# Optimization experiments

Hardware: AMD Instinct MI355X
Metric: run time of the kernel (lower is better)

## Reference

```python
import jax, jax.numpy as jnp
import numpy as np

N = 50000          # nodes per type (assmpt=0, non_assmpt=1, rule=2)
E = 400000         # edges per relation
# (src_type, dst_type) for the 9 relations in the module's dict order
REL = [(0, 2), (1, 2), (1, 0), (0, 0), (2, 1), (2, 0), (0, 0), (2, 2), (1, 1)]


def setup_inputs() -> dict:
    key = jax.random.key(0)
    ks = jax.random.split(key, 8)
    inp = {
        "x_assmpt": jax.random.normal(ks[0], (N, 128), jnp.float32),
        "x_non_assmpt": jax.random.normal(ks[1], (N, 128), jnp.float32),
        "x_rule": jax.random.normal(ks[2], (N, 128), jnp.float32),
        "W1": jax.random.normal(ks[3], (9, 128, 128), jnp.float32) * 0.06,
        "b1": jnp.zeros((9, 128), jnp.float32),
        "W2": jax.random.normal(ks[4], (9, 128, 128), jnp.float32) * 0.06,
        "b2": jnp.zeros((9, 128), jnp.float32),
        "Wc": jax.random.normal(ks[5], (128, 16), jnp.float32) * 0.08,
        "bc": jnp.zeros((16,), jnp.float32),
        "edges": jax.random.randint(ks[6], (9, 2, E), 0, N, jnp.int32),
    }
    return inp


def _hetero_layer(xs, edges, W, b):
    """One HeteroGraphConv layer (DGL GraphConv, norm='both', aggregate='sum').
    xs: list of 3 [N, din]; W: [9, din, dout]; b: [9, dout]. Returns list of 3 [N, dout]."""
    dout = W.shape[2]
    outs = [jnp.zeros((N, dout), xs[0].dtype) for _ in range(3)]
    for r, (s, d) in enumerate(REL):
        src, dst = edges[r, 0], edges[r, 1]
        ones = jnp.ones((E,), xs[0].dtype)
        out_deg = jax.ops.segment_sum(ones, src, num_segments=N)   # src out-degree
        in_deg = jax.ops.segment_sum(ones, dst, num_segments=N)    # dst in-degree
        norm_s = jnp.where(out_deg > 0, out_deg, 1.0) ** -0.5
        norm_s = jnp.where(out_deg > 0, norm_s, 0.0)
        norm_d = jnp.where(in_deg > 0, in_deg, 1.0) ** -0.5
        norm_d = jnp.where(in_deg > 0, norm_d, 0.0)
        h = (xs[s] * norm_s[:, None]) @ W[r]                       # [N, dout] project first
        agg = jax.ops.segment_sum(h[src], dst, num_segments=N)     # SpMM gather/scatter
        outs[d] = outs[d] + agg * norm_d[:, None] + b[r]
    return outs


def reference(x_assmpt, x_non_assmpt, x_rule, W1, b1, W2, b2, Wc, bc, edges):
    xs = [x_assmpt, x_non_assmpt, x_rule]
    h = _hetero_layer(xs, edges, W1, b1)
    h = [jax.nn.relu(v) for v in h]
    h = _hetero_layer(h, edges, W2, b2)
    h = [jax.nn.relu(v) for v in h]
    h = [v @ Wc + bc for v in h]
    return jnp.stack(h, axis=0)  # [3, N, out] : (assmpt, non_assmpt, rule)
```

## Files before the change

kernel.cpp:

```cpp
#include <hip/hip_runtime.h>
#include <hip/hip_bf16.h>
#include <hip/hip_fp16.h>


#define NN 50000
#define EE 400000
#define NRG 4
#define RGN (NN / NRG)
#define HCH 16
#define HEG (EE / HCH)
#define NBK 98
#define BKW 512
#define CH1 8192
#define NCH ((EE + CH1 - 1) / CH1)
#define SCAP 6656

typedef __attribute__((ext_vector_type(8))) _Float16 f16x8;
typedef __attribute__((ext_vector_type(4))) float f32x4;
#define MFMAH(a, b, c) __builtin_amdgcn_mfma_f32_16x16x32_f16(a, b, c, 0, 0, 0)

__global__ __launch_bounds__(256) void k_hist(const int* __restrict__ edges,
                                              unsigned* __restrict__ hist) {
    __shared__ unsigned bins[RGN / 2];
    int bid = blockIdx.x;
    int r = bid >> 6;
    int rem = bid & 63;
    int rg = rem >> 4;
    int c = rem & 15;
    int tid = threadIdx.x;
    for (int i = tid; i < RGN / 2; i += 256) bins[i] = 0;
    __syncthreads();
    const int* ea = edges + (size_t)r * 2 * EE + (size_t)c * HEG;
    int base = rg * RGN;
    for (int e = tid; e < HEG; e += 256) {
        int idx = __builtin_nontemporal_load(&ea[e]) - base;
        if ((unsigned)idx < (unsigned)RGN)
            atomicAdd(&bins[idx >> 1], (idx & 1) ? 65536u : 1u);
    }
    __syncthreads();
    unsigned* ho = hist + ((size_t)(r * NRG + rg) * HCH + c) * (RGN / 2);
    for (int i = tid; i < RGN / 2; i += 256) ho[i] = bins[i];
}

__global__ void k_sums(const unsigned* __restrict__ hist, float* __restrict__ ns) {
    int i = blockIdx.x * blockDim.x + threadIdx.x;
    if (i >= 9 * (NN / 2)) return;
    int r = i / (NN / 2);
    int ps = i - r * (NN / 2);
    int rg = ps / (RGN / 2);
    int slot = ps - rg * (RGN / 2);
    const unsigned* hs = hist + ((size_t)(r * NRG + rg) * HCH) * (RGN / 2) + slot;
    unsigned slo = 0, shi = 0;
#pragma unroll
    for (int c = 0; c < HCH; ++c) {
        unsigned a = hs[(size_t)c * (RGN / 2)];
        slo += a & 0xffffu; shi += a >> 16;
    }
    int n0 = 2 * ps;
    ns[r * NN + n0]     = slo ? rsqrtf((float)slo) : 0.f;
    ns[r * NN + n0 + 1] = shi ? rsqrtf((float)shi) : 0.f;
}

__global__ __launch_bounds__(256) void k_bcount(const int* __restrict__ edges,
                                                int* __restrict__ bcount) {
    __shared__ int bins[NBK];
    int bid = blockIdx.x;
    int r = bid / NCH, c = bid - r * NCH;
    int tid = threadIdx.x;
    for (int i = tid; i < NBK; i += 256) bins[i] = 0;
    __syncthreads();
    int e0 = c * CH1, e1 = min(EE, e0 + CH1);
    const int* ed = edges + (size_t)r * 2 * EE + EE;
    for (int e = e0 + tid; e < e1; e += 256)
        atomicAdd(&bins[__builtin_nontemporal_load(&ed[e]) >> 9], 1);
    __syncthreads();
    for (int i = tid; i < NBK; i += 256)
        if (bins[i]) atomicAdd(&bcount[r * NBK + i], bins[i]);
}

__global__ void k_bscan(const int* __restrict__ bcount, int* __restrict__ bbase,
                        int* __restrict__ gcur, int* __restrict__ off) {
    int r = threadIdx.x;
    if (r >= 9) return;
    int acc = 0;
    for (int b = 0; b < NBK; ++b) {
        bbase[r * (NBK + 1) + b] = acc;
        gcur[r * NBK + b] = acc;
        acc += bcount[r * NBK + b];
    }
    bbase[r * (NBK + 1) + NBK] = acc;
    off[r * (NN + 1) + NN] = acc;
}

__global__ __launch_bounds__(256) void k_bucket(const int* __restrict__ edges,
                                                int* __restrict__ gcur,
                                                unsigned* __restrict__ bpairs) {
    __shared__ int hist[NBK];
    __shared__ int sc[128];
    __shared__ int lofs[NBK + 1];
    __shared__ int lcur[NBK];
    __shared__ int gbase[NBK];
    __shared__ unsigned stage[CH1];
    int bid = blockIdx.x;
    int r = bid / NCH, c = bid - r * NCH;
    int tid = threadIdx.x;
    int e0 = c * CH1;
    int e1 = min(EE, e0 + CH1);
    int n = e1 - e0;
    const int* es = edges + (size_t)r * 2 * EE;
    const int* ed = es + EE;

    for (int i = tid; i < NBK; i += 256) hist[i] = 0;
    __syncthreads();
    for (int e = e0 + tid; e < e1; e += 256)
        atomicAdd(&hist[ed[e] >> 9], 1);
    __syncthreads();
    if (tid < 128) sc[tid] = (tid < NBK) ? hist[tid] : 0;
    __syncthreads();
#pragma unroll
    for (int s = 1; s < 128; s <<= 1) {
        int t = 0;
        if (tid < 128 && tid >= s) t = sc[tid - s];
        __syncthreads();
        if (tid < 128 && tid >= s) sc[tid] += t;
        __syncthreads();
    }
    if (tid < NBK) {
        int ex = sc[tid] - hist[tid];
        lofs[tid] = ex;
        lcur[tid] = ex;
        gbase[tid] = atomicAdd(&gcur[r * NBK + tid], hist[tid]);
    }
    if (tid == 0) lofs[NBK] = n;
    __syncthreads();
    for (int e = e0 + tid; e < e1; e += 256) {
        int dst = ed[e];
        int src = es[e];
        int p = atomicAdd(&lcur[dst >> 9], 1);
        stage[p] = ((unsigned)dst << 16) | (unsigned)src;
    }
    __syncthreads();
    unsigned* bp = bpairs + (size_t)r * EE;
    for (int i = tid; i < n; i += 256) {
        int lo = 0, hi = NBK;
        while (hi - lo > 1) {
            int m = (lo + hi) >> 1;
            if (lofs[m] <= i) lo = m; else hi = m;
        }
        bp[gbase[lo] + (i - lofs[lo])] = stage[i];
    }
}

__global__ __launch_bounds__(256) void k_scatter(const unsigned* __restrict__ bpairs,
                                                 const int* __restrict__ bbase,
                                                 int* __restrict__ off,
                                                 float* __restrict__ nd,
                                                 int* __restrict__ esrc) {
    __shared__ int bins[BKW];
    __shared__ int lcur[BKW];
    __shared__ int wsum[4];
    __shared__ int lout[SCAP];
    int bid = blockIdx.x;
    int r = bid / NBK, b = bid - r * NBK;
    int tid = threadIdx.x;
    int d0 = b * BKW;
    int d1 = min(NN, d0 + BKW);
    int nb = d1 - d0;
    int s0 = bbase[r * (NBK + 1) + b];
    int s1 = bbase[r * (NBK + 1) + b + 1];
    int n = s1 - s0;
    for (int i = tid; i < BKW; i += 256) bins[i] = 0;
    __syncthreads();
    const unsigned* bp = bpairs + (size_t)r * EE + s0;
    for (int i = tid; i < n; i += 256)
        atomicAdd(&bins[(int)(bp[i] >> 16) - d0], 1);
    __syncthreads();
    int v0 = bins[2 * tid], v1 = bins[2 * tid + 1];
    int s = v0 + v1;
    int lane = tid & 63, w = tid >> 6;
    int x = s;
#pragma unroll
    for (int sh = 1; sh < 64; sh <<= 1) {
        int y = __shfl_up(x, (unsigned)sh);
        if (lane >= sh) x += y;
    }
    if (lane == 63) wsum[w] = x;
    __syncthreads();
    int wb = 0;
#pragma unroll
    for (int j = 0; j < 3; ++j) wb += (j < w) ? wsum[j] : 0;
    int ex = wb + x - s;
    int* o = off + r * (NN + 1);
    if (2 * tid < nb) {
        o[d0 + 2 * tid] = s0 + ex;
        nd[r * NN + d0 + 2 * tid] = v0 ? rsqrtf((float)v0) : 0.f;
    }
    if (2 * tid + 1 < nb) {
        o[d0 + 2 * tid + 1] = s0 + ex + v0;
        nd[r * NN + d0 + 2 * tid + 1] = v1 ? rsqrtf((float)v1) : 0.f;
    }
    lcur[2 * tid] = ex;
    lcur[2 * tid + 1] = ex + v0;
    __syncthreads();
    int* out = esrc + (size_t)r * EE + s0;
    if (n <= SCAP) {
        for (int i = tid; i < n; i += 256) {
            unsigned pr = bp[i];
            int p = atomicAdd(&lcur[(int)(pr >> 16) - d0], 1);
            lout[p] = (int)(pr & 0xffffu);
        }
        __syncthreads();
        for (int i = tid; i < n; i += 256) out[i] = lout[i];
    } else {
        for (int i = tid; i < n; i += 256) {
            unsigned pr = bp[i];
            int p = atomicAdd(&lcur[(int)(pr >> 16) - d0], 1);
            out[p] = (int)(pr & 0xffffu);
        }
    }
}

__global__ void k_xprep(const float* __restrict__ x0, const float* __restrict__ x1,
                        const float* __restrict__ x2, __half* __restrict__ xh) {
    int i = blockIdx.x * blockDim.x + threadIdx.x;
    const int per = NN * 32;
    if (i >= 3 * per) return;
    int tsel = i / per;
    int o = i - tsel * per;
    const float* xp = (tsel == 0) ? x0 : ((tsel == 1) ? x1 : x2);
    float4 v = *reinterpret_cast<const float4*>(xp + (size_t)o * 4);
    __half* dst = xh + (size_t)tsel * NN * 128 + (size_t)o * 4;
    *reinterpret_cast<__half2*>(dst) = __floats2half2_rn(v.x, v.y);
    *reinterpret_cast<__half2*>(dst + 2) = __floats2half2_rn(v.z, v.w);
}

__global__ void k_wprep(const float* __restrict__ W1, const float* __restrict__ W2,
                        __half* __restrict__ whi) {
    int id = blockIdx.x * blockDim.x + threadIdx.x;
    const int total = 2 * 9 * 128 * 128;
    if (id >= total) return;
    int n = id & 127;
    int k = (id >> 7) & 127;
    int rl = id >> 14;
    const float* W = (rl < 9) ? W1 : W2;
    int r = (rl < 9) ? rl : rl - 9;
    float f = W[((size_t)r * 128 + k) * 128 + n];
    size_t oidx = (((size_t)rl * 4 + (k >> 5)) * 128 + n) * 32 + (k & 31);
    whi[oidx] = __float2half_rn(f);
}

struct AggT {
    const __half* xin;
    const int* off;
    const int* esrc;
    const float* ns;
    const float* nd;
    __half* A;
};

template <int RELU>
__global__ __launch_bounds__(256) void k_agg3(AggT t0, AggT t1, AggT t2) {
    int bid = blockIdx.x;
    int task = bid % 3;
    AggT t = (task == 0) ? t0 : ((task == 1) ? t1 : t2);
    int wave = (bid / 3) * 4 + (threadIdx.x >> 6);
    int lane = threadIdx.x & 63;
    if (wave >= NN) return;
    int g = lane >> 4;
    int c = lane & 15;
    int e0 = t.off[wave], e1 = t.off[wave + 1];
    const __half* xin = t.xin;
    const int* esrc = t.esrc;
    const float* ns = t.ns;
    float acc[8] = {};
    for (int e = e0; e < e1; e += 8) {
        int ea = e + g;
        int eb = e + 4 + g;
        bool va = ea < e1, vb = eb < e1;
        int sa = va ? esrc[ea] : esrc[e];
        int sb = vb ? esrc[eb] : esrc[e];
        float wa = va ? ns[sa] : 0.f;
        float wb = vb ? ns[sb] : 0.f;
        float4 ra = *reinterpret_cast<const float4*>(xin + (size_t)sa * 128 + c * 8);
        float4 rb = *reinterpret_cast<const float4*>(xin + (size_t)sb * 128 + c * 8);
        const __half2* pa = reinterpret_cast<const __half2*>(&ra);
        const __half2* pb = reinterpret_cast<const __half2*>(&rb);
#pragma unroll
        for (int j = 0; j < 4; ++j) {
            float2 fa = __half22float2(pa[j]);
            float2 fb = __half22float2(pb[j]);
            if (RELU) {
                fa.x = fmaxf(fa.x, 0.f); fa.y = fmaxf(fa.y, 0.f);
                fb.x = fmaxf(fb.x, 0.f); fb.y = fmaxf(fb.y, 0.f);
            }
            acc[2 * j]     = fmaf(wa, fa.x, acc[2 * j]);
            acc[2 * j + 1] = fmaf(wa, fa.y, acc[2 * j + 1]);
            acc[2 * j]     = fmaf(wb, fb.x, acc[2 * j]);
            acc[2 * j + 1] = fmaf(wb, fb.y, acc[2 * j + 1]);
        }
    }
#pragma unroll
    for (int j = 0; j < 8; ++j) {
        acc[j] += __shfl_xor(acc[j], 16);
        acc[j] += __shfl_xor(acc[j], 32);
    }
    if (g == 0) {
        float nr = t.nd[wave];
        f16x8 hv;
#pragma unroll
        for (int j = 0; j < 8; ++j) hv[j] = (_Float16)(acc[j] * nr);
        *reinterpret_cast<f16x8*>(t.A + (size_t)wave * 128 + c * 8) = hv;
    }
}

template <int NS, int STORE>
__global__ __launch_bounds__(256) void k_gemm_mfma(
    const __half* __restrict__ Aa, const __half* __restrict__ Ab,
    const __half* __restrict__ wha, const __half* __restrict__ whb,
    const float* __restrict__ ba, const float* __restrict__ bb,
    __half* __restrict__ H) {
    int tid = threadIdx.x;
    int w = tid >> 6, lane = tid & 63;
    int row0 = blockIdx.x * 64;
    int colbase = w * 32;
    int r16 = lane & 15;
    int koff = (lane >> 4) * 8;

    f32x4 acc[4][2];
#pragma unroll
    for (int rt = 0; rt < 4; ++rt)
#pragma unroll
        for (int nt = 0; nt < 2; ++nt)
            acc[rt][nt] = f32x4{0.f, 0.f, 0.f, 0.f};

#pragma unroll
    for (int s = 0; s < NS; ++s) {
        const __half* A = (s == 0) ? Aa : Ab;
        const __half* w_h = (s == 0) ? wha : whb;
#pragma unroll
        for (int c = 0; c < 4; ++c) {
            int kbase = c * 32 + koff;
            f16x8 av[4], bh[2];
#pragma unroll
            for (int rt = 0; rt < 4; ++rt) {
                int rr = rt * 16 + r16;
                int rc = (row0 + rr < NN) ? rr : 0;
                av[rt] = *reinterpret_cast<const f16x8*>(
                    A + ((size_t)(row0 + rc)) * 128 + kbase);
            }
#pragma unroll
            for (int nt = 0; nt < 2; ++nt) {
                int col = colbase + nt * 16 + r16;
                size_t widx = ((size_t)c * 128 + col) * 32 + koff;
                bh[nt] = *reinterpret_cast<const f16x8*>(w_h + widx);
            }
#pragma unroll
            for (int rt = 0; rt < 4; ++rt)
#pragma unroll
                for (int nt = 0; nt < 2; ++nt)
                    acc[rt][nt] = MFMAH(av[rt], bh[nt], acc[rt][nt]);
        }
    }

    int orow = (lane >> 4) * 4;
#pragma unroll
    for (int nt = 0; nt < 2; ++nt) {
        int col = colbase + nt * 16 + r16;
        float bias = ba[col];
        if (NS == 2) bias += bb[col];
#pragma unroll
        for (int rt = 0; rt < 4; ++rt) {
#pragma unroll
            for (int j = 0; j < 4; ++j) {
                int grow = row0 + rt * 16 + orow + j;
                if (grow < NN) {
                    __half* hp = H + (size_t)grow * 128 + col;
                    float v = acc[rt][nt][j] + bias;
                    if (!STORE) v += __half2float(*hp);
                    *hp = __float2half_rn(v);
                }
            }
        }
    }
}

__global__ __launch_bounds__(256) void k_classifier(const __half* __restrict__ H,
                                                    const float* __restrict__ Wc,
                                                    const float* __restrict__ bc,
                                                    float* __restrict__ out) {
    __shared__ float sW[128 * 16];
    __shared__ float sb[16];
    int tid = threadIdx.x;
#pragma unroll
    for (int i = tid; i < 2048; i += 256) sW[i] = Wc[i];
    if (tid < 16) sb[tid] = bc[tid];
    __syncthreads();
    int node = blockIdx.x * 64 + (tid >> 2);
    if (node >= 3 * NN) return;
    int cg = (tid & 3) << 2;
    const __half* h = H + (size_t)node * 128;
    float acc0 = 0.f, acc1 = 0.f, acc2 = 0.f, acc3 = 0.f;
#pragma unroll 2
    for (int k0 = 0; k0 < 128; k0 += 8) {
        float4 raw = *reinterpret_cast<const float4*>(h + k0);
        const __half2* hp2 = reinterpret_cast<const __half2*>(&raw);
#pragma unroll
        for (int jj = 0; jj < 4; ++jj) {
            float2 f = __half22float2(hp2[jj]);
            float a;
            a = fmaxf(f.x, 0.f);
            { float4 wv = *reinterpret_cast<const float4*>(&sW[(k0 + 2 * jj) * 16 + cg]);
              acc0 = fmaf(a, wv.x, acc0); acc1 = fmaf(a, wv.y, acc1);
              acc2 = fmaf(a, wv.z, acc2); acc3 = fmaf(a, wv.w, acc3); }
            a = fmaxf(f.y, 0.f);
            { float4 wv = *reinterpret_cast<const float4*>(&sW[(k0 + 2 * jj + 1) * 16 + cg]);
              acc0 = fmaf(a, wv.x, acc0); acc1 = fmaf(a, wv.y, acc1);
              acc2 = fmaf(a, wv.z, acc2); acc3 = fmaf(a, wv.w, acc3); }
        }
    }
    float4 o = make_float4(acc0 + sb[cg], acc1 + sb[cg + 1],
                           acc2 + sb[cg + 2], acc3 + sb[cg + 3]);
    *reinterpret_cast<float4*>(out + (size_t)node * 16 + cg) = o;
}

extern "C" void kernel_launch(void* const* d_in, const int* in_sizes, int n_in,
                              void* d_out, int out_size, void* d_ws, size_t ws_size,
                              hipStream_t stream) {
    const float* x0 = (const float*)d_in[0];
    const float* x1 = (const float*)d_in[1];
    const float* x2 = (const float*)d_in[2];
    const float* W1 = (const float*)d_in[3];
    const float* b1 = (const float*)d_in[4];
    const float* W2 = (const float*)d_in[5];
    const float* b2 = (const float*)d_in[6];
    const float* Wc = (const float*)d_in[7];
    const float* bc = (const float*)d_in[8];
    const int* edges = (const int*)d_in[9];

    char* p = (char*)d_ws;
    auto alloc = [&](size_t bytes) -> void* {
        void* r = (void*)p;
        p += (bytes + 255) & ~(size_t)255;
        return r;
    };
    __half* h2h = (__half*)alloc((size_t)3 * NN * 128 * sizeof(__half));
    unsigned* hist = (unsigned*)h2h;
    unsigned* bpairs = (unsigned*)h2h;
    __half* xh  = (__half*)alloc((size_t)3 * NN * 128 * sizeof(__half));
    __half* h1h = (__half*)alloc((size_t)3 * NN * 128 * sizeof(__half));
    __half* A6  = (__half*)alloc((size_t)6 * NN * 128 * sizeof(__half));
    int* off = (int*)alloc((size_t)9 * (NN + 1) * sizeof(int));
    float* ns = (float*)alloc((size_t)9 * NN * sizeof(float));
    float* nd = (float*)alloc((size_t)9 * NN * sizeof(float));
    int* esrc = (int*)alloc((size_t)9 * EE * sizeof(int));
    __half* whi = (__half*)alloc((size_t)2 * 9 * 128 * 128 * sizeof(__half));
    int* gcur = (int*)alloc((size_t)9 * NBK * sizeof(int));
    int* bcount = (int*)alloc((size_t)9 * NBK * sizeof(int));
    int* bbase = (int*)alloc((size_t)9 * (NBK + 1) * sizeof(int));
    __half* P[6];
    for (int j = 0; j < 6; ++j) P[j] = A6 + (size_t)j * NN * 128;
    const __half* xph[3] = {xh, xh + (size_t)NN * 128, xh + (size_t)2 * NN * 128};

    k_hist<<<9 * NRG * HCH, 256, 0, stream>>>(edges, hist);
    k_xprep<<<(3 * NN * 32 + 255) / 256, 256, 0, stream>>>(x0, x1, x2, xh);
    k_sums<<<(9 * (NN / 2) + 255) / 256, 256, 0, stream>>>(hist, ns);
    hipMemsetAsync(bcount, 0, (size_t)9 * NBK * sizeof(int), stream);
    k_bcount<<<9 * NCH, 256, 0, stream>>>(edges, bcount);
    k_bscan<<<1, 64, 0, stream>>>(bcount, bbase, gcur, off);
    k_bucket<<<9 * NCH, 256, 0, stream>>>(edges, gcur, bpairs);
    k_scatter<<<9 * NBK, 256, 0, stream>>>(bpairs, bbase, off, nd, esrc);
    k_wprep<<<(2 * 9 * 128 * 128 + 255) / 256, 256, 0, stream>>>(W1, W2, whi);

    const int agg_grid = 3 * 12500;
    const int gemm_blocks = (NN + 63) / 64;

    auto mk = [&](int r, const __half* xin, __half* slot) -> AggT {
        return AggT{xin, off + r * (NN + 1), esrc + (size_t)r * EE,
                    ns + r * NN, nd + r * NN, slot};
    };
    auto wp = [&](int layer, int r) { return (size_t)(layer * 9 + r) * 16384; };

    for (int L = 0; L < 2; ++L) {
        const float* b = (L == 0) ? b1 : b2;
        __half* o0 = ((L == 0) ? h1h : h2h) + (size_t)0 * NN * 128;
        __half* o1 = ((L == 0) ? h1h : h2h) + (size_t)1 * NN * 128;
        __half* o2 = ((L == 0) ? h1h : h2h) + (size_t)2 * NN * 128;
        const __half* in0 = (L == 0) ? xph[0] : h1h + (size_t)0 * NN * 128;
        const __half* in1 = (L == 0) ? xph[1] : h1h + (size_t)1 * NN * 128;
        const __half* in2 = (L == 0) ? xph[2] : h1h + (size_t)2 * NN * 128;

        if (L == 0)
            k_agg3<0><<<agg_grid, 256, 0, stream>>>(mk(0, in0, P[0]), mk(3, in0, P[1]),
                                                    mk(6, in0, P[2]));
        else
            k_agg3<1><<<agg_grid, 256, 0, stream>>>(mk(0, in0, P[0]), mk(3, in0, P[1]),
                                                    mk(6, in0, P[2]));
        k_gemm_mfma<2, 1><<<gemm_blocks, 256, 0, stream>>>(
            P[1], P[2], whi + wp(L, 3), whi + wp(L, 6),
            b + 3 * 128, b + 6 * 128, o0);
        k_gemm_mfma<1, 1><<<gemm_blocks, 256, 0, stream>>>(
            P[0], P[0], whi + wp(L, 0), whi + wp(L, 0),
            b + 0 * 128, b + 0 * 128, o2);

        if (L == 0)
            k_agg3<0><<<agg_grid, 256, 0, stream>>>(mk(1, in1, P[3]), mk(2, in1, P[4]),
                                                    mk(8, in1, P[5]));
        else
            k_agg3<1><<<agg_grid, 256, 0, stream>>>(mk(1, in1, P[3]), mk(2, in1, P[4]),
                                                    mk(8, in1, P[5]));
        if (L == 0)
            k_agg3<0><<<agg_grid, 256, 0, stream>>>(mk(4, in2, P[0]), mk(5, in2, P[1]),
                                                    mk(7, in2, P[2]));
        else
            k_agg3<1><<<agg_grid, 256, 0, stream>>>(mk(4, in2, P[0]), mk(5, in2, P[1]),
                                                    mk(7, in2, P[2]));

        k_gemm_mfma<2, 1><<<gemm_blocks, 256, 0, stream>>>(
            P[5], P[0], whi + wp(L, 8), whi + wp(L, 4),
            b + 8 * 128, b + 4 * 128, o1);
        k_gemm_mfma<2, 0><<<gemm_blocks, 256, 0, stream>>>(
            P[4], P[1], whi + wp(L, 2), whi + wp(L, 5),
            b + 2 * 128, b + 5 * 128, o0);
        k_gemm_mfma<2, 0><<<gemm_blocks, 256, 0, stream>>>(
            P[3], P[2], whi + wp(L, 1), whi + wp(L, 7),
            b + 1 * 128, b + 7 * 128, o2);
    }

    k_classifier<<<(3 * NN + 63) / 64, 256, 0, stream>>>(h2h, Wc, bc, (float*)d_out);
}
```

Measured before the change: 798.4 us.

## Pack fp16 source norm into edge list and accumulate aggregation in packed half

The CSR build step now writes, for each edge, the source index together with its fp16 source-normalisation weight in one 32-bit word, so the aggregation kernel no longer does a dependent gather of ns[src]. The aggregation loop processes 16 edges per iteration with four independent packed-half accumulators, using packed fp16 FMA and max instead of converting to fp32. This is meant to cut dependent memory latency and ALU work in the dominant gather kernel. In exchange, the source norm and the running sums are kept in fp16, which reduces accuracy for high-degree nodes, and the packing relies on node indices fitting in 16 bits.

```diff
diff --git a/kernel.cpp b/kernel.cpp
--- a/kernel.cpp
+++ b/kernel.cpp
@@ -16,6 +16,7 @@
 #define SCAP 6656
 
 typedef __attribute__((ext_vector_type(8))) _Float16 f16x8;
+typedef __attribute__((ext_vector_type(2))) _Float16 h2f;
 typedef __attribute__((ext_vector_type(4))) float f32x4;
 #define MFMAH(a, b, c) __builtin_amdgcn_mfma_f32_16x16x32_f16(a, b, c, 0, 0, 0)
 
@@ -42,7 +43,7 @@
     for (int i = tid; i < RGN / 2; i += 256) ho[i] = bins[i];
 }
 
-__global__ void k_sums(const unsigned* __restrict__ hist, float* __restrict__ ns) {
+__global__ void k_sums(const unsigned* __restrict__ hist, __half* __restrict__ nsh) {
     int i = blockIdx.x * blockDim.x + threadIdx.x;
     if (i >= 9 * (NN / 2)) return;
     int r = i / (NN / 2);
@@ -57,8 +58,8 @@
         slo += a & 0xffffu; shi += a >> 16;
     }
     int n0 = 2 * ps;
-    ns[r * NN + n0]     = slo ? rsqrtf((float)slo) : 0.f;
-    ns[r * NN + n0 + 1] = shi ? rsqrtf((float)shi) : 0.f;
+    nsh[r * NN + n0]     = slo ? __float2half_rn(rsqrtf((float)slo)) : __half(0.f);
+    nsh[r * NN + n0 + 1] = shi ? __float2half_rn(rsqrtf((float)shi)) : __half(0.f);
 }
 
 __global__ __launch_bounds__(256) void k_bcount(const int* __restrict__ edges,
@@ -153,13 +154,14 @@
 
 __global__ __launch_bounds__(256) void k_scatter(const unsigned* __restrict__ bpairs,
                                                  const int* __restrict__ bbase,
+                                                 const __half* __restrict__ nsh,
                                                  int* __restrict__ off,
                                                  float* __restrict__ nd,
-                                                 int* __restrict__ esrc) {
+                                                 unsigned* __restrict__ esn) {
     __shared__ int bins[BKW];
     __shared__ int lcur[BKW];
     __shared__ int wsum[4];
-    __shared__ int lout[SCAP];
+    __shared__ unsigned lout[SCAP];
     int bid = blockIdx.x;
     int r = bid / NBK, b = bid - r * NBK;
     int tid = threadIdx.x;
@@ -202,20 +204,25 @@
     lcur[2 * tid] = ex;
     lcur[2 * tid + 1] = ex + v0;
     __syncthreads();
-    int* out = esrc + (size_t)r * EE + s0;
+    const __half* nsr = nsh + (size_t)r * NN;
+    unsigned* out = esn + (size_t)r * EE + s0;
     if (n <= SCAP) {
         for (int i = tid; i < n; i += 256) {
             unsigned pr = bp[i];
+            int src = (int)(pr & 0xffffu);
+            unsigned wbits = (unsigned)__half_as_ushort(nsr[src]);
             int p = atomicAdd(&lcur[(int)(pr >> 16) - d0], 1);
-            lout[p] = (int)(pr & 0xffffu);
+            lout[p] = (wbits << 16) | (unsigned)src;
         }
         __syncthreads();
         for (int i = tid; i < n; i += 256) out[i] = lout[i];
     } else {
         for (int i = tid; i < n; i += 256) {
             unsigned pr = bp[i];
+            int src = (int)(pr & 0xffffu);
+            unsigned wbits = (unsigned)__half_as_ushort(nsr[src]);
             int p = atomicAdd(&lcur[(int)(pr >> 16) - d0], 1);
-            out[p] = (int)(pr & 0xffffu);
+            out[p] = (wbits << 16) | (unsigned)src;
         }
     }
 }
@@ -252,8 +259,7 @@
 struct AggT {
     const __half* xin;
     const int* off;
-    const int* esrc;
-    const float* ns;
+    const unsigned* esn;
     const float* nd;
     __half* A;
 };
@@ -270,34 +276,55 @@
     int c = lane & 15;
     int e0 = t.off[wave], e1 = t.off[wave + 1];
     const __half* xin = t.xin;
-    const int* esrc = t.esrc;
-    const float* ns = t.ns;
-    float acc[8] = {};
-    for (int e = e0; e < e1; e += 8) {
-        int ea = e + g;
-        int eb = e + 4 + g;
-        bool va = ea < e1, vb = eb < e1;
-        int sa = va ? esrc[ea] : esrc[e];
-        int sb = vb ? esrc[eb] : esrc[e];
-        float wa = va ? ns[sa] : 0.f;
-        float wb = vb ? ns[sb] : 0.f;
+    const unsigned* esn = t.esn;
+    const h2f zz = {(_Float16)0.f, (_Float16)0.f};
+    h2f accA[4] = {zz, zz, zz, zz};
+    h2f accB[4] = {zz, zz, zz, zz};
+    h2f accC[4] = {zz, zz, zz, zz};
+    h2f accD[4] = {zz, zz, zz, zz};
+    for (int e = e0; e < e1; e += 16) {
+        int ea = e + g, eb = e + 4 + g, ec = e + 8 + g, ed = e + 12 + g;
+        bool va = ea < e1, vb = eb < e1, vc = ec < e1, vd = ed < e1;
+        unsigned ua = esn[va ? ea : e];
+        unsigned ub = esn[vb ? eb : e];
+        unsigned uc = esn[vc ? ec : e];
+        unsigned ud = esn[vd ? ed : e];
+        int sa = ua & 0xffffu, sb = ub & 0xffffu, sc_ = uc & 0xffffu, sd = ud & 0xffffu;
+        _Float16 wa = va ? __builtin_bit_cast(_Float16, (unsigned short)(ua >> 16)) : (_Float16)0.f;
+        _Float16 wb = vb ? __builtin_bit_cast(_Float16, (unsigned short)(ub >> 16)) : (_Float16)0.f;
+        _Float16 wc = vc ? __builtin_bit_cast(_Float16, (unsigned short)(uc >> 16)) : (_Float16)0.f;
+        _Float16 wd = vd ? __builtin_bit_cast(_Float16, (unsigned short)(ud >> 16)) : (_Float16)0.f;
+        h2f wav = {wa, wa}, wbv = {wb, wb}, wcv = {wc, wc}, wdv = {wd, wd};
         float4 ra = *reinterpret_cast<const float4*>(xin + (size_t)sa * 128 + c * 8);
         float4 rb = *reinterpret_cast<const float4*>(xin + (size_t)sb * 128 + c * 8);
-        const __half2* pa = reinterpret_cast<const __half2*>(&ra);
-        const __half2* pb = reinterpret_cast<const __half2*>(&rb);
+        float4 rc = *reinterpret_cast<const float4*>(xin + (size_t)sc_ * 128 + c * 8);
+        float4 rd = *reinterpret_cast<const float4*>(xin + (size_t)sd * 128 + c * 8);
+        const h2f* pa = reinterpret_cast<const h2f*>(&ra);
+        const h2f* pb = reinterpret_cast<const h2f*>(&rb);
+        const h2f* pc = reinterpret_cast<const h2f*>(&rc);
+        const h2f* pd = reinterpret_cast<const h2f*>(&rd);
 #pragma unroll
         for (int j = 0; j < 4; ++j) {
-            float2 fa = __half22float2(pa[j]);
-            float2 fb = __half22float2(pb[j]);
+            h2f fa = pa[j], fb = pb[j], fc = pc[j], fd = pd[j];
             if (RELU) {
-                fa.x = fmaxf(fa.x, 0.f); fa.y = fmaxf(fa.y, 0.f);
-                fb.x = fmaxf(fb.x, 0.f); fb.y = fmaxf(fb.y, 0.f);
+                fa = __builtin_elementwise_max(fa, zz);
+                fb = __builtin_elementwise_max(fb, zz);
+                fc = __builtin_elementwise_max(fc, zz);
+                fd = __builtin_elementwise_max(fd, zz);
             }
-            acc[2 * j]     = fmaf(wa, fa.x, acc[2 * j]);
-            acc[2 * j + 1] = fmaf(wa, fa.y, acc[2 * j + 1]);
-            acc[2 * j]     = fmaf(wb, fb.x, acc[2 * j]);
-            acc[2 * j + 1] = fmaf(wb, fb.y, acc[2 * j + 1]);
-        }
+            accA[j] = wav * fa + accA[j];
+            accB[j] = wbv * fb + accB[j];
+            accC[j] = wcv * fc + accC[j];
+            accD[j] = wdv * fd + accD[j];
+        }
+    }
+    float acc[8];
+#pragma unroll
+    for (int j = 0; j < 4; ++j) {
+        acc[2 * j]     = ((float)accA[j][0] + (float)accB[j][0]) +
+                         ((float)accC[j][0] + (float)accD[j][0]);
+        acc[2 * j + 1] = ((float)accA[j][1] + (float)accB[j][1]) +
+                         ((float)accC[j][1] + (float)accD[j][1]);
     }
 #pragma unroll
     for (int j = 0; j < 8; ++j) {
@@ -450,9 +477,9 @@
     __half* h1h = (__half*)alloc((size_t)3 * NN * 128 * sizeof(__half));
     __half* A6  = (__half*)alloc((size_t)6 * NN * 128 * sizeof(__half));
     int* off = (int*)alloc((size_t)9 * (NN + 1) * sizeof(int));
-    float* ns = (float*)alloc((size_t)9 * NN * sizeof(float));
+    __half* nsh = (__half*)alloc((size_t)9 * NN * sizeof(__half));
     float* nd = (float*)alloc((size_t)9 * NN * sizeof(float));
-    int* esrc = (int*)alloc((size_t)9 * EE * sizeof(int));
+    unsigned* esn = (unsigned*)alloc((size_t)9 * EE * sizeof(unsigned));
     __half* whi = (__half*)alloc((size_t)2 * 9 * 128 * 128 * sizeof(__half));
     int* gcur = (int*)alloc((size_t)9 * NBK * sizeof(int));
     int* bcount = (int*)alloc((size_t)9 * NBK * sizeof(int));
@@ -463,20 +490,20 @@
 
     k_hist<<<9 * NRG * HCH, 256, 0, stream>>>(edges, hist);
     k_xprep<<<(3 * NN * 32 + 255) / 256, 256, 0, stream>>>(x0, x1, x2, xh);
-    k_sums<<<(9 * (NN / 2) + 255) / 256, 256, 0, stream>>>(hist, ns);
+    k_sums<<<(9 * (NN / 2) + 255) / 256, 256, 0, stream>>>(hist, nsh);
     hipMemsetAsync(bcount, 0, (size_t)9 * NBK * sizeof(int), stream);
     k_bcount<<<9 * NCH, 256, 0, stream>>>(edges, bcount);
     k_bscan<<<1, 64, 0, stream>>>(bcount, bbase, gcur, off);
     k_bucket<<<9 * NCH, 256, 0, stream>>>(edges, gcur, bpairs);
-    k_scatter<<<9 * NBK, 256, 0, stream>>>(bpairs, bbase, off, nd, esrc);
+    k_scatter<<<9 * NBK, 256, 0, stream>>>(bpairs, bbase, nsh, off, nd, esn);
     k_wprep<<<(2 * 9 * 128 * 128 + 255) / 256, 256, 0, stream>>>(W1, W2, whi);
 
     const int agg_grid = 3 * 12500;
     const int gemm_blocks = (NN + 63) / 64;
 
     auto mk = [&](int r, const __half* xin, __half* slot) -> AggT {
-        return AggT{xin, off + r * (NN + 1), esrc + (size_t)r * EE,
-                    ns + r * NN, nd + r * NN, slot};
+        return AggT{xin, off + r * (NN + 1), esn + (size_t)r * EE,
+                    nd + r * NN, slot};
     };
     auto wp = [&](int layer, int r) { return (size_t)(layer * 9 + r) * 16384; };
 
```

Measured after the change: 753.5 us. 1.06x faster.
